# Optimization experiments

Measured on AMD Instinct MI355X. Metric: run time of the kernel, lower is better.

The kernel has to match this reference:

```python
import jax, jax.numpy as jnp
import numpy as np

D_IN = 1024
D_OUT = 1024
NUM_HEADS = 16
HEAD_DIM = D_OUT // NUM_HEADS


def setup_inputs() -> dict:
    key = jax.random.key(0)
    ks = jax.random.split(key, 6)
    scale = 0.02
    x = jax.random.normal(ks[0], (4, 2048, D_IN), dtype=jnp.float32)
    Wq = jax.random.normal(ks[1], (D_IN, D_OUT), dtype=jnp.float32) * scale
    Wk = jax.random.normal(ks[2], (D_IN, D_OUT), dtype=jnp.float32) * scale
    Wv = jax.random.normal(ks[3], (D_IN, D_OUT), dtype=jnp.float32) * scale
    Wo = jax.random.normal(ks[4], (D_OUT, D_OUT), dtype=jnp.float32) * scale
    bo = jax.random.normal(ks[5], (D_OUT,), dtype=jnp.float32) * scale
    return {"x": x, "Wq": Wq, "Wk": Wk, "Wv": Wv, "Wo": Wo, "bo": bo}


def reference(x, Wq, Wk, Wv, Wo, bo):
    b, n, _ = x.shape
    # QKV projections -> [b, h, n, hd]
    def split_heads(t):
        return t.reshape(b, n, NUM_HEADS, HEAD_DIM).transpose(0, 2, 1, 3)
    q = split_heads(x @ Wq)
    k = split_heads(x @ Wk)
    v = split_heads(x @ Wv)
    # scaled causal attention scores [b, h, n, n]
    scores = jnp.einsum('bhqd,bhkd->bhqk', q, k) / jnp.sqrt(jnp.float32(HEAD_DIM))
    causal = jnp.tril(jnp.ones((n, n), dtype=bool))
    scores = jnp.where(causal, scores, -jnp.inf)
    attn = jax.nn.softmax(scores, axis=-1)
    # dropout p=0.0 -> identity
    ctx = jnp.einsum('bhqk,bhkd->bhqd', attn, v)  # [b, h, n, hd]
    ctx = ctx.transpose(0, 2, 1, 3).reshape(b, n, D_OUT)
    return ctx @ Wo + bo
```

## Files before the change

### kernel.cpp

```cpp
#include <hip/hip_runtime.h>
#include <hip/hip_bf16.h>

typedef __bf16 bf16;
typedef __attribute__((ext_vector_type(8))) __bf16 bf16x8;
typedef __attribute__((ext_vector_type(4))) __bf16 bf16x4;
typedef __attribute__((ext_vector_type(4))) float floatx4;

#define DM 1024
#define NH 16
#define HD 64
#define SEQ 2048
#define BATCH 4
#define MTOT (BATCH * SEQ)

#define GLDS(g, l) \
  __builtin_amdgcn_global_load_lds((const __attribute__((address_space(1))) void*)(g), \
                                   (__attribute__((address_space(3))) void*)(l), 16, 0, 0)

__global__ void cvt_f32_bf16(const float* __restrict__ in, bf16* __restrict__ out, int n4) {
  int i = blockIdx.x * 256 + threadIdx.x;
  if (i < n4) {
    float4 v = ((const float4*)in)[i];
    bf16x4 o;
    o[0] = (bf16)v.x; o[1] = (bf16)v.y; o[2] = (bf16)v.z; o[3] = (bf16)v.w;
    ((bf16x4*)out)[i] = o;
  }
}

__global__ void transpose_cvt4(const float* __restrict__ Wq, const float* __restrict__ Wk,
                               const float* __restrict__ Wv, const float* __restrict__ Wo,
                               bf16* __restrict__ Wqkvt, bf16* __restrict__ Wot) {
  __shared__ float tile[32][33];
  const float* W;
  bf16* Wt;
  int z = blockIdx.z;
  if (z == 0) { W = Wq; Wt = Wqkvt; }
  else if (z == 1) { W = Wk; Wt = Wqkvt + (size_t)DM * DM; }
  else if (z == 2) { W = Wv; Wt = Wqkvt + (size_t)2 * DM * DM; }
  else { W = Wo; Wt = Wot; }
  int n0 = blockIdx.x * 32, k0 = blockIdx.y * 32;
  int tx = threadIdx.x, ty = threadIdx.y;
#pragma unroll
  for (int j = 0; j < 32; j += 8)
    tile[ty + j][tx] = W[(size_t)(k0 + ty + j) * DM + n0 + tx];
  __syncthreads();
#pragma unroll
  for (int j = 0; j < 32; j += 8)
    Wt[(size_t)(n0 + ty + j) * DM + k0 + tx] = (bf16)tile[tx][ty + j];
}

#define BK 64

__global__ __launch_bounds__(256, 3) void gemm_qkv(const bf16* __restrict__ A,
                                                   const bf16* __restrict__ Bt,
                                                   bf16* __restrict__ Qb,
                                                   bf16* __restrict__ Kb,
                                                   bf16* __restrict__ Vt) {
  __shared__ __align__(16) bf16 Alds[128 * BK];
  __shared__ __align__(16) bf16 Blds[128 * BK];
  const int K = 1024;
  int m0 = blockIdx.x * 128;
  int n0 = blockIdx.y * 128;
  int tid = threadIdx.x;
  int wave = tid >> 6, lane = tid & 63;
  int wm = (wave & 1) * 64, wn = (wave >> 1) * 64;
  int lm = lane & 15, quad = lane >> 4;
  int lm7 = lm & 7;

  int cbase = wave * 64 + lane;
  const bf16* gA[4];
  const bf16* gB[4];
  bf16 *lA[4], *lB[4];
#pragma unroll
  for (int seg = 0; seg < 4; ++seg) {
    int c = seg * 256 + cbase;
    int row = c >> 3;
    int col8 = (c & 7) ^ (row & 7);
    gA[seg] = A + (size_t)(m0 + row) * K + col8 * 8;
    gB[seg] = Bt + (size_t)(n0 + row) * K + col8 * 8;
    lA[seg] = Alds + c * 8;
    lB[seg] = Blds + c * 8;
  }

  floatx4 acc[4][4] = {};
  for (int kt = 0; kt < K; kt += BK) {
    __syncthreads();
#pragma unroll
    for (int seg = 0; seg < 4; ++seg) {
      GLDS(gA[seg] + kt, lA[seg]);
      GLDS(gB[seg] + kt, lB[seg]);
    }
    __syncthreads();
#pragma unroll
    for (int ks = 0; ks < 2; ++ks) {
      int xk = (ks * 4 + quad) ^ lm7;
      bf16x8 af[4], bfr[4];
#pragma unroll
      for (int t = 0; t < 4; ++t) {
        af[t] = *(const bf16x8*)(Alds + (wm + t * 16 + lm) * BK + xk * 8);
        bfr[t] = *(const bf16x8*)(Blds + (wn + t * 16 + lm) * BK + xk * 8);
      }
#pragma unroll
      for (int i = 0; i < 4; ++i)
#pragma unroll
        for (int j = 0; j < 4; ++j)
          acc[i][j] = __builtin_amdgcn_mfma_f32_16x16x32_bf16(af[i], bfr[j], acc[i][j], 0, 0, 0);
    }
  }
#pragma unroll
  for (int i = 0; i < 4; ++i) {
#pragma unroll
    for (int j = 0; j < 4; ++j) {
#pragma unroll
      for (int r = 0; r < 4; ++r) {
        int R = m0 + wm + i * 16 + quad * 4 + r;
        int C = n0 + wn + j * 16 + lm;
        int b = R >> 11, n = R & 2047;
        int proj = C >> 10, c = C & 1023;
        int h = c >> 6, d = c & 63;
        int bh = b * NH + h;
        bf16 bv = (bf16)acc[i][j][r];
        if (proj == 0)
          Qb[((size_t)bh * SEQ + n) * HD + d] = bv;
        else if (proj == 1)
          Kb[((size_t)bh * SEQ + n) * HD + d] = bv;
        else
          Vt[((size_t)bh * HD + d) * SEQ + n] = bv;
      }
    }
  }
}

__global__ __launch_bounds__(256, 3) void gemm_out(const bf16* __restrict__ A,
                                                   const bf16* __restrict__ Bt,
                                                   const float* __restrict__ bias,
                                                   float* __restrict__ out) {
  __shared__ __align__(16) bf16 Alds[128 * BK];
  __shared__ __align__(16) bf16 Blds[128 * BK];
  const int K = 1024;
  int m0 = blockIdx.x * 128;
  int n0 = blockIdx.y * 128;
  int tid = threadIdx.x;
  int wave = tid >> 6, lane = tid & 63;
  int wm = (wave & 1) * 64, wn = (wave >> 1) * 64;
  int lm = lane & 15, quad = lane >> 4;
  int lm7 = lm & 7;

  int cbase = wave * 64 + lane;
  const bf16* gA[4];
  const bf16* gB[4];
  bf16 *lA[4], *lB[4];
#pragma unroll
  for (int seg = 0; seg < 4; ++seg) {
    int c = seg * 256 + cbase;
    int row = c >> 3;
    int col8 = (c & 7) ^ (row & 7);
    gA[seg] = A + (size_t)(m0 + row) * K + col8 * 8;
    gB[seg] = Bt + (size_t)(n0 + row) * K + col8 * 8;
    lA[seg] = Alds + c * 8;
    lB[seg] = Blds + c * 8;
  }

  floatx4 acc[4][4] = {};
  for (int kt = 0; kt < K; kt += BK) {
    __syncthreads();
#pragma unroll
    for (int seg = 0; seg < 4; ++seg) {
      GLDS(gA[seg] + kt, lA[seg]);
      GLDS(gB[seg] + kt, lB[seg]);
    }
    __syncthreads();
#pragma unroll
    for (int ks = 0; ks < 2; ++ks) {
      int xk = (ks * 4 + quad) ^ lm7;
      bf16x8 af[4], bfr[4];
#pragma unroll
      for (int t = 0; t < 4; ++t) {
        af[t] = *(const bf16x8*)(Alds + (wm + t * 16 + lm) * BK + xk * 8);
        bfr[t] = *(const bf16x8*)(Blds + (wn + t * 16 + lm) * BK + xk * 8);
      }
#pragma unroll
      for (int i = 0; i < 4; ++i)
#pragma unroll
        for (int j = 0; j < 4; ++j)
          acc[i][j] = __builtin_amdgcn_mfma_f32_16x16x32_bf16(af[i], bfr[j], acc[i][j], 0, 0, 0);
    }
  }
#pragma unroll
  for (int i = 0; i < 4; ++i)
#pragma unroll
    for (int j = 0; j < 4; ++j)
#pragma unroll
      for (int r = 0; r < 4; ++r) {
        int R = m0 + wm + i * 16 + quad * 4 + r;
        int C = n0 + wn + j * 16 + lm;
        out[(size_t)R * DM + C] = acc[i][j][r] + bias[C];
      }
}

#define SKV 72

__global__ __launch_bounds__(256) void attn(const bf16* __restrict__ Qb,
                                            const bf16* __restrict__ Kb,
                                            const bf16* __restrict__ Vt,
                                            bf16* __restrict__ ctx) {
  __shared__ __align__(16) bf16 Klds[64 * SKV];
  __shared__ __align__(16) bf16 Vlds[64 * SKV];
  int blk = blockIdx.x;
  int xcd = blk & 7;
  int k = blk >> 3;
  int p = k & 15;
  int bh = (k >> 4) * 8 + xcd;
  int tid = threadIdx.x, wave = tid >> 6, lane = tid & 63;
  int lm = lane & 15, quad = lane >> 4;
  const bf16* Qp = Qb + (size_t)bh * SEQ * HD;
  const bf16* Kp = Kb + (size_t)bh * SEQ * HD;
  const bf16* Vp = Vt + (size_t)bh * HD * SEQ;
  int sr = tid >> 3, sc = (tid & 7) * 8;
  int b = bh >> 4, h = bh & 15;

#pragma unroll 1
  for (int phase = 0; phase < 2; ++phase) {
    int qt = phase ? (31 - p) : p;
    int q0 = qt * 64;
    int rowbase = q0 + wave * 16;

    bf16x8 qf[2];
#pragma unroll
    for (int ks = 0; ks < 2; ++ks) {
      bf16x8 q = *(const bf16x8*)(Qp + (size_t)(rowbase + lm) * HD + ks * 32 + quad * 8);
#pragma unroll
      for (int j = 0; j < 8; ++j) q[j] = (bf16)((float)q[j] * 0.125f);
      qf[ks] = q;
    }

    floatx4 acco[4] = {};
    float lsum = 0.f;
    int nkv = qt + 1;

    bf16x8 ka0 = *(const bf16x8*)(Kp + (size_t)sr * HD + sc);
    bf16x8 ka1 = *(const bf16x8*)(Kp + (size_t)(32 + sr) * HD + sc);
    bf16x8 va0 = *(const bf16x8*)(Vp + (size_t)sr * SEQ + sc);
    bf16x8 va1 = *(const bf16x8*)(Vp + (size_t)(32 + sr) * SEQ + sc);
    __syncthreads();
    *(bf16x8*)(Klds + sr * SKV + sc) = ka0;
    *(bf16x8*)(Klds + (32 + sr) * SKV + sc) = ka1;
    *(bf16x8*)(Vlds + sr * SKV + sc) = va0;
    *(bf16x8*)(Vlds + (32 + sr) * SKV + sc) = va1;

#pragma unroll 1
    for (int t = 0; t < nkv; ++t) {
      __syncthreads();
      int kv0 = t * 64;
      if (t + 1 < nkv) {
        int kn = kv0 + 64;
        ka0 = *(const bf16x8*)(Kp + (size_t)(kn + sr) * HD + sc);
        ka1 = *(const bf16x8*)(Kp + (size_t)(kn + 32 + sr) * HD + sc);
        va0 = *(const bf16x8*)(Vp + (size_t)sr * SEQ + kn + sc);
        va1 = *(const bf16x8*)(Vp + (size_t)(32 + sr) * SEQ + kn + sc);
      }

      floatx4 st[4] = {};
#pragma unroll
      for (int mt = 0; mt < 4; ++mt) {
        bf16x8 kf0 = *(const bf16x8*)(Klds + (mt * 16 + lm) * SKV + quad * 8);
        bf16x8 kf1 = *(const bf16x8*)(Klds + (mt * 16 + lm) * SKV + 32 + quad * 8);
        st[mt] = __builtin_amdgcn_mfma_f32_16x16x32_bf16(kf0, qf[0], st[mt], 0, 0, 0);
        st[mt] = __builtin_amdgcn_mfma_f32_16x16x32_bf16(kf1, qf[1], st[mt], 0, 0, 0);
      }

      bf16x4 pb[4];
      if (t != qt) {
#pragma unroll
        for (int mt = 0; mt < 4; ++mt)
#pragma unroll
          for (int r = 0; r < 4; ++r) {
            float pv = __expf(st[mt][r]);
            lsum += pv;
            pb[mt][r] = (bf16)pv;
          }
      } else {
        int qrel = wave * 16 + lm;
#pragma unroll
        for (int mt = 0; mt < 4; ++mt)
#pragma unroll
          for (int r = 0; r < 4; ++r) {
            float pv = __expf(st[mt][r]);
            if (mt * 16 + quad * 4 + r > qrel) pv = 0.f;
            lsum += pv;
            pb[mt][r] = (bf16)pv;
          }
      }

#pragma unroll
      for (int ks = 0; ks < 2; ++ks) {
        bf16x8 pf;
#pragma unroll
        for (int j = 0; j < 4; ++j) { pf[j] = pb[2 * ks][j]; pf[4 + j] = pb[2 * ks + 1][j]; }
#pragma unroll
        for (int db = 0; db < 4; ++db) {
          const bf16* vrow = Vlds + (db * 16 + lm) * SKV + ks * 32 + quad * 4;
          bf16x4 v0 = *(const bf16x4*)(vrow);
          bf16x4 v1 = *(const bf16x4*)(vrow + 16);
          bf16x8 vf;
#pragma unroll
          for (int j = 0; j < 4; ++j) { vf[j] = v0[j]; vf[4 + j] = v1[j]; }
          acco[db] = __builtin_amdgcn_mfma_f32_16x16x32_bf16(vf, pf, acco[db], 0, 0, 0);
        }
      }

      if (t + 1 < nkv) {
        __syncthreads();
        *(bf16x8*)(Klds + sr * SKV + sc) = ka0;
        *(bf16x8*)(Klds + (32 + sr) * SKV + sc) = ka1;
        *(bf16x8*)(Vlds + sr * SKV + sc) = va0;
        *(bf16x8*)(Vlds + (32 + sr) * SKV + sc) = va1;
      }
    }

    lsum += __shfl_xor(lsum, 16, 64);
    lsum += __shfl_xor(lsum, 32, 64);
    float linv = 1.0f / lsum;

    bf16* crow = ctx + ((size_t)b * SEQ + rowbase + lm) * DM + h * 64;
#pragma unroll
    for (int db = 0; db < 4; ++db) {
      bf16x4 o;
#pragma unroll
      for (int r = 0; r < 4; ++r) o[r] = (bf16)(acco[db][r] * linv);
      *(bf16x4*)(crow + db * 16 + quad * 4) = o;
    }
  }
}

extern "C" void kernel_launch(void* const* d_in, const int* in_sizes, int n_in,
                              void* d_out, int out_size, void* d_ws, size_t ws_size,
                              hipStream_t stream) {
  const float* x = (const float*)d_in[0];
  const float* Wq = (const float*)d_in[1];
  const float* Wk = (const float*)d_in[2];
  const float* Wv = (const float*)d_in[3];
  const float* Wo = (const float*)d_in[4];
  const float* bo = (const float*)d_in[5];
  float* out = (float*)d_out;

  bf16* ws = (bf16*)d_ws;
  bf16* xb = ws;
  bf16* Wqkvt = xb + (size_t)MTOT * DM;
  bf16* Wot = Wqkvt + (size_t)3 * DM * DM;
  bf16* Qb = Wot + (size_t)DM * DM;
  bf16* Kb = Qb + (size_t)BATCH * NH * SEQ * HD;
  bf16* Vtb = Kb + (size_t)BATCH * NH * SEQ * HD;
  bf16* ctx = xb;

  cvt_f32_bf16<<<(MTOT * DM / 4 + 255) / 256, 256, 0, stream>>>(x, xb, MTOT * DM / 4);
  transpose_cvt4<<<dim3(32, 32, 4), dim3(32, 8), 0, stream>>>(Wq, Wk, Wv, Wo, Wqkvt, Wot);
  gemm_qkv<<<dim3(MTOT / 128, 3 * DM / 128), 256, 0, stream>>>(xb, Wqkvt, Qb, Kb, Vtb);
  attn<<<1024, 256, 0, stream>>>(Qb, Kb, Vtb, ctx);
  gemm_out<<<dim3(MTOT / 128, DM / 128), 256, 0, stream>>>(ctx, Wot, bo, out);
}
```

Measured before the change: 255.6 us.

## Enlarge attention query tile to 128 rows with MFMA-based row sums

Each attention block now handles 128 query rows (32 per wave, two 16-row MFMA tiles) instead of 64, so every K/V tile staged in LDS is reused by twice as many queries and the grid is halved. The softmax exponent moves to exp2 with log2e folded into the Q scale, and row sums are accumulated through an extra MFMA against a ones vector instead of scalar adds and shuffles. Waves whose rows are entirely before a KV tile skip its compute. The trade-off is more registers per wave, fewer blocks for load balancing, and idle waves on diagonal tiles.

```diff
diff --git a/kernel.cpp b/kernel.cpp
--- a/kernel.cpp
+++ b/kernel.cpp
@@ -209,8 +209,8 @@
   int blk = blockIdx.x;
   int xcd = blk & 7;
   int k = blk >> 3;
-  int p = k & 15;
-  int bh = (k >> 4) * 8 + xcd;
+  int p = k & 7;
+  int bh = (k >> 3) * 8 + xcd;
   int tid = threadIdx.x, wave = tid >> 6, lane = tid & 63;
   int lm = lane & 15, quad = lane >> 4;
   const bf16* Qp = Qb + (size_t)bh * SEQ * HD;
@@ -218,25 +218,35 @@
   const bf16* Vp = Vt + (size_t)bh * HD * SEQ;
   int sr = tid >> 3, sc = (tid & 7) * 8;
   int b = bh >> 4, h = bh & 15;
+  const float QSCALE = 0.125f * 1.4426950408889634f;
+
+  bf16x8 ones;
+#pragma unroll
+  for (int j = 0; j < 8; ++j) ones[j] = (lm == 0) ? (bf16)1.0f : (bf16)0.0f;
 
 #pragma unroll 1
   for (int phase = 0; phase < 2; ++phase) {
-    int qt = phase ? (31 - p) : p;
-    int q0 = qt * 64;
-    int rowbase = q0 + wave * 16;
-
-    bf16x8 qf[2];
-#pragma unroll
-    for (int ks = 0; ks < 2; ++ks) {
-      bf16x8 q = *(const bf16x8*)(Qp + (size_t)(rowbase + lm) * HD + ks * 32 + quad * 8);
-#pragma unroll
-      for (int j = 0; j < 8; ++j) q[j] = (bf16)((float)q[j] * 0.125f);
-      qf[ks] = q;
-    }
-
-    floatx4 acco[4] = {};
-    float lsum = 0.f;
-    int nkv = qt + 1;
+    int qt = phase ? (15 - p) : p;
+    int q0 = qt * 128;
+    int rowbase = q0 + wave * 32;
+
+    bf16x8 qfA[2], qfB[2];
+#pragma unroll
+    for (int ks2 = 0; ks2 < 2; ++ks2) {
+      bf16x8 qa = *(const bf16x8*)(Qp + (size_t)(rowbase + lm) * HD + ks2 * 32 + quad * 8);
+      bf16x8 qb = *(const bf16x8*)(Qp + (size_t)(rowbase + 16 + lm) * HD + ks2 * 32 + quad * 8);
+#pragma unroll
+      for (int j = 0; j < 8; ++j) {
+        qa[j] = (bf16)((float)qa[j] * QSCALE);
+        qb[j] = (bf16)((float)qb[j] * QSCALE);
+      }
+      qfA[ks2] = qa;
+      qfB[ks2] = qb;
+    }
+
+    floatx4 accA[4] = {}, accB[4] = {};
+    floatx4 aclA = {}, aclB = {};
+    int nkv = 2 * qt + 2;
 
     bf16x8 ka0 = *(const bf16x8*)(Kp + (size_t)sr * HD + sc);
     bf16x8 ka1 = *(const bf16x8*)(Kp + (size_t)(32 + sr) * HD + sc);
@@ -260,52 +270,65 @@
         va1 = *(const bf16x8*)(Vp + (size_t)(32 + sr) * SEQ + kn + sc);
       }
 
-      floatx4 st[4] = {};
-#pragma unroll
-      for (int mt = 0; mt < 4; ++mt) {
-        bf16x8 kf0 = *(const bf16x8*)(Klds + (mt * 16 + lm) * SKV + quad * 8);
-        bf16x8 kf1 = *(const bf16x8*)(Klds + (mt * 16 + lm) * SKV + 32 + quad * 8);
-        st[mt] = __builtin_amdgcn_mfma_f32_16x16x32_bf16(kf0, qf[0], st[mt], 0, 0, 0);
-        st[mt] = __builtin_amdgcn_mfma_f32_16x16x32_bf16(kf1, qf[1], st[mt], 0, 0, 0);
-      }
-
-      bf16x4 pb[4];
-      if (t != qt) {
-#pragma unroll
-        for (int mt = 0; mt < 4; ++mt)
-#pragma unroll
-          for (int r = 0; r < 4; ++r) {
-            float pv = __expf(st[mt][r]);
-            lsum += pv;
-            pb[mt][r] = (bf16)pv;
+      if (kv0 <= rowbase + 31) {
+        floatx4 stA[4] = {}, stB[4] = {};
+#pragma unroll
+        for (int mt = 0; mt < 4; ++mt) {
+          bf16x8 kf0 = *(const bf16x8*)(Klds + (mt * 16 + lm) * SKV + quad * 8);
+          bf16x8 kf1 = *(const bf16x8*)(Klds + (mt * 16 + lm) * SKV + 32 + quad * 8);
+          stA[mt] = __builtin_amdgcn_mfma_f32_16x16x32_bf16(kf0, qfA[0], stA[mt], 0, 0, 0);
+          stA[mt] = __builtin_amdgcn_mfma_f32_16x16x32_bf16(kf1, qfA[1], stA[mt], 0, 0, 0);
+          stB[mt] = __builtin_amdgcn_mfma_f32_16x16x32_bf16(kf0, qfB[0], stB[mt], 0, 0, 0);
+          stB[mt] = __builtin_amdgcn_mfma_f32_16x16x32_bf16(kf1, qfB[1], stB[mt], 0, 0, 0);
+        }
+
+        bf16x4 pbA[4], pbB[4];
+        if (kv0 + 63 <= rowbase) {
+#pragma unroll
+          for (int mt = 0; mt < 4; ++mt)
+#pragma unroll
+            for (int r = 0; r < 4; ++r) {
+              pbA[mt][r] = (bf16)exp2f(stA[mt][r]);
+              pbB[mt][r] = (bf16)exp2f(stB[mt][r]);
+            }
+        } else {
+          int qrelA = rowbase - kv0 + lm;
+          int qrelB = qrelA + 16;
+#pragma unroll
+          for (int mt = 0; mt < 4; ++mt)
+#pragma unroll
+            for (int r = 0; r < 4; ++r) {
+              int kvrel = mt * 16 + quad * 4 + r;
+              float pa = exp2f(stA[mt][r]);
+              float pbv = exp2f(stB[mt][r]);
+              if (kvrel > qrelA) pa = 0.f;
+              if (kvrel > qrelB) pbv = 0.f;
+              pbA[mt][r] = (bf16)pa;
+              pbB[mt][r] = (bf16)pbv;
+            }
+        }
+
+#pragma unroll
+        for (int ks = 0; ks < 2; ++ks) {
+          bf16x8 pfA, pfB;
+#pragma unroll
+          for (int j = 0; j < 4; ++j) {
+            pfA[j] = pbA[2 * ks][j]; pfA[4 + j] = pbA[2 * ks + 1][j];
+            pfB[j] = pbB[2 * ks][j]; pfB[4 + j] = pbB[2 * ks + 1][j];
           }
-      } else {
-        int qrel = wave * 16 + lm;
-#pragma unroll
-        for (int mt = 0; mt < 4; ++mt)
-#pragma unroll
-          for (int r = 0; r < 4; ++r) {
-            float pv = __expf(st[mt][r]);
-            if (mt * 16 + quad * 4 + r > qrel) pv = 0.f;
-            lsum += pv;
-            pb[mt][r] = (bf16)pv;
+          aclA = __builtin_amdgcn_mfma_f32_16x16x32_bf16(ones, pfA, aclA, 0, 0, 0);
+          aclB = __builtin_amdgcn_mfma_f32_16x16x32_bf16(ones, pfB, aclB, 0, 0, 0);
+#pragma unroll
+          for (int db = 0; db < 4; ++db) {
+            const bf16* vrow = Vlds + (db * 16 + lm) * SKV + ks * 32 + quad * 4;
+            bf16x4 v0 = *(const bf16x4*)(vrow);
+            bf16x4 v1 = *(const bf16x4*)(vrow + 16);
+            bf16x8 vf;
+#pragma unroll
+            for (int j = 0; j < 4; ++j) { vf[j] = v0[j]; vf[4 + j] = v1[j]; }
+            accA[db] = __builtin_amdgcn_mfma_f32_16x16x32_bf16(vf, pfA, accA[db], 0, 0, 0);
+            accB[db] = __builtin_amdgcn_mfma_f32_16x16x32_bf16(vf, pfB, accB[db], 0, 0, 0);
           }
-      }
-
-#pragma unroll
-      for (int ks = 0; ks < 2; ++ks) {
-        bf16x8 pf;
-#pragma unroll
-        for (int j = 0; j < 4; ++j) { pf[j] = pb[2 * ks][j]; pf[4 + j] = pb[2 * ks + 1][j]; }
-#pragma unroll
-        for (int db = 0; db < 4; ++db) {
-          const bf16* vrow = Vlds + (db * 16 + lm) * SKV + ks * 32 + quad * 4;
-          bf16x4 v0 = *(const bf16x4*)(vrow);
-          bf16x4 v1 = *(const bf16x4*)(vrow + 16);
-          bf16x8 vf;
-#pragma unroll
-          for (int j = 0; j < 4; ++j) { vf[j] = v0[j]; vf[4 + j] = v1[j]; }
-          acco[db] = __builtin_amdgcn_mfma_f32_16x16x32_bf16(vf, pf, acco[db], 0, 0, 0);
         }
       }
 
@@ -318,17 +341,21 @@
       }
     }
 
-    lsum += __shfl_xor(lsum, 16, 64);
-    lsum += __shfl_xor(lsum, 32, 64);
-    float linv = 1.0f / lsum;
-
-    bf16* crow = ctx + ((size_t)b * SEQ + rowbase + lm) * DM + h * 64;
+    float linvA = 1.0f / __shfl(aclA[0], lm, 64);
+    float linvB = 1.0f / __shfl(aclB[0], lm, 64);
+
+    bf16* crowA = ctx + ((size_t)b * SEQ + rowbase + lm) * DM + h * 64;
+    bf16* crowB = crowA + (size_t)16 * DM;
 #pragma unroll
     for (int db = 0; db < 4; ++db) {
-      bf16x4 o;
-#pragma unroll
-      for (int r = 0; r < 4; ++r) o[r] = (bf16)(acco[db][r] * linv);
-      *(bf16x4*)(crow + db * 16 + quad * 4) = o;
+      bf16x4 oa, ob;
+#pragma unroll
+      for (int r = 0; r < 4; ++r) {
+        oa[r] = (bf16)(accA[db][r] * linvA);
+        ob[r] = (bf16)(accB[db][r] * linvB);
+      }
+      *(bf16x4*)(crowA + db * 16 + quad * 4) = oa;
+      *(bf16x4*)(crowB + db * 16 + quad * 4) = ob;
     }
   }
 }
@@ -356,6 +383,6 @@
   cvt_f32_bf16<<<(MTOT * DM / 4 + 255) / 256, 256, 0, stream>>>(x, xb, MTOT * DM / 4);
   transpose_cvt4<<<dim3(32, 32, 4), dim3(32, 8), 0, stream>>>(Wq, Wk, Wv, Wo, Wqkvt, Wot);
   gemm_qkv<<<dim3(MTOT / 128, 3 * DM / 128), 256, 0, stream>>>(xb, Wqkvt, Qb, Kb, Vtb);
-  attn<<<1024, 256, 0, stream>>>(Qb, Kb, Vtb, ctx);
+  attn<<<512, 256, 0, stream>>>(Qb, Kb, Vtb, ctx);
   gemm_out<<<dim3(MTOT / 128, DM / 128), 256, 0, stream>>>(ctx, Wot, bo, out);
 }
```

Measured after the change: 293.1 us. 14.7% more time.
